# Kernel tuning notes

Hardware: AMD Instinct MI355X
Metric: run time of the kernel (lower is better)

Reference implementation:

```python
import jax, jax.numpy as jnp
import numpy as np
from jax import lax

B, T, N = 512, 512, 64  # batch, max_seq_len, num_tags


def setup_inputs() -> dict:
    key = jax.random.key(0)
    k1, k2, k3, k4 = jax.random.split(key, 4)
    inputs = jax.random.normal(k1, (B, T, N), dtype=jnp.float32)
    transition_params = jax.random.normal(k2, (N, N), dtype=jnp.float32)
    tag_indices = jax.random.randint(k3, (B, T), 0, N, dtype=jnp.int32)
    sequence_lengths = jax.random.randint(k4, (B,), 0, T, dtype=jnp.int32)
    return {
        "inputs": inputs,
        "transition_params": transition_params,
        "tag_indices": tag_indices,
        "sequence_lengths": sequence_lengths,
    }


def _crf_log_norm(inputs, transition_params, sequence_lengths):
    # inputs: [B, T, N]
    first = inputs[:, 0, :]                       # alpha after first token, [B, N]
    rest = jnp.transpose(inputs[:, 1:, :], (1, 0, 2))  # [T-1, B, N]

    def step(alpha, emit):
        # alpha: [B, N] -> broadcast-add transitions [N, N], logsumexp over prev tag
        new = emit + jax.nn.logsumexp(alpha[:, :, None] + transition_params[None], axis=1)
        return new, new

    _, alphas = lax.scan(step, first, rest)       # [T-1, B, N]
    all_alphas = jnp.concatenate([first[None], alphas], axis=0)  # [T, B, N]
    all_alphas = jnp.transpose(all_alphas, (1, 0, 2))            # [B, T, N]
    last_index = jnp.maximum(0, sequence_lengths - 1)            # [B]
    alpha_last = jnp.take_along_axis(all_alphas, last_index[:, None, None], axis=1)[:, 0, :]
    return jax.nn.logsumexp(alpha_last, axis=1)   # [B]


def _crf_sequence_score(inputs, tag_indices, sequence_lengths, transition_params):
    mask = (jnp.arange(T)[None, :] < sequence_lengths[:, None]).astype(inputs.dtype)  # [B, T]
    # unary: gather emission score of the gold tag at each position
    unary = jnp.take_along_axis(inputs, tag_indices[:, :, None], axis=2)[:, :, 0]      # [B, T]
    unary_scores = jnp.sum(unary * mask, axis=1)
    # binary: transition scores between consecutive gold tags
    binary = transition_params[tag_indices[:, :-1], tag_indices[:, 1:]]                # [B, T-1]
    binary_scores = jnp.sum(binary * mask[:, 1:], axis=1)
    return unary_scores + binary_scores


def reference(inputs, transition_params, tag_indices, sequence_lengths):
    tag_indices = tag_indices.astype(jnp.int32)
    sequence_lengths = sequence_lengths.astype(jnp.int32)
    sequence_scores = _crf_sequence_score(inputs, tag_indices, sequence_lengths, transition_params)
    log_norm = _crf_log_norm(inputs, transition_params, sequence_lengths)
    log_likelihood = sequence_scores - log_norm   # [B]
    return (log_likelihood, transition_params)
```

## Files before the change

kernel.cpp:

```cpp
#include <hip/hip_runtime.h>

#define BB 512
#define TT 512
#define NN 64

__device__ __forceinline__ float readlane_f(float v, int lane) {
    return __int_as_float(__builtin_amdgcn_readlane(__float_as_int(v), lane));
}

template<int BASE>
__device__ __forceinline__ float dot16(float p, const float4& A, const float4& B,
                                       const float4& C, const float4& D) {
    float s0 = readlane_f(p, BASE + 0) * A.x;
    float s1 = readlane_f(p, BASE + 1) * A.y;
    float s2 = readlane_f(p, BASE + 2) * A.z;
    float s3 = readlane_f(p, BASE + 3) * A.w;
    s0 = fmaf(readlane_f(p, BASE + 4),  B.x, s0);
    s1 = fmaf(readlane_f(p, BASE + 5),  B.y, s1);
    s2 = fmaf(readlane_f(p, BASE + 6),  B.z, s2);
    s3 = fmaf(readlane_f(p, BASE + 7),  B.w, s3);
    s0 = fmaf(readlane_f(p, BASE + 8),  C.x, s0);
    s1 = fmaf(readlane_f(p, BASE + 9),  C.y, s1);
    s2 = fmaf(readlane_f(p, BASE + 10), C.z, s2);
    s3 = fmaf(readlane_f(p, BASE + 11), C.w, s3);
    s0 = fmaf(readlane_f(p, BASE + 12), D.x, s0);
    s1 = fmaf(readlane_f(p, BASE + 13), D.y, s1);
    s2 = fmaf(readlane_f(p, BASE + 14), D.z, s2);
    s3 = fmaf(readlane_f(p, BASE + 15), D.w, s3);
    return (s0 + s1) + (s2 + s3);
}

template<int BASE>
__device__ __forceinline__ float run_loop(const float* __restrict__ inb,
                                          const float* __restrict__ trans,
                                          int last, int j, float alpha,
                                          float (*pbuf)[4][NN]) {
    constexpr int W = BASE / 16;

    float4 E0, E1, E2, E3;
    E0.x = __expf(trans[(BASE + 0) * NN + j]);
    E0.y = __expf(trans[(BASE + 1) * NN + j]);
    E0.z = __expf(trans[(BASE + 2) * NN + j]);
    E0.w = __expf(trans[(BASE + 3) * NN + j]);
    E1.x = __expf(trans[(BASE + 4) * NN + j]);
    E1.y = __expf(trans[(BASE + 5) * NN + j]);
    E1.z = __expf(trans[(BASE + 6) * NN + j]);
    E1.w = __expf(trans[(BASE + 7) * NN + j]);
    E2.x = __expf(trans[(BASE + 8) * NN + j]);
    E2.y = __expf(trans[(BASE + 9) * NN + j]);
    E2.z = __expf(trans[(BASE + 10) * NN + j]);
    E2.w = __expf(trans[(BASE + 11) * NN + j]);
    E3.x = __expf(trans[(BASE + 12) * NN + j]);
    E3.y = __expf(trans[(BASE + 13) * NN + j]);
    E3.z = __expf(trans[(BASE + 14) * NN + j]);
    E3.w = __expf(trans[(BASE + 15) * NN + j]);

    for (int t0 = 1; t0 <= last; t0 += 16) {
        float4 pf0, pf1, pf2, pf3;
#define LDE(vec, comp, r) { const int tc = (t0 + (r) <= last) ? (t0 + (r)) : last; \
                            vec.comp = inb[tc * NN + j]; }
        LDE(pf0, x, 0)  LDE(pf0, y, 1)  LDE(pf0, z, 2)  LDE(pf0, w, 3)
        LDE(pf1, x, 4)  LDE(pf1, y, 5)  LDE(pf1, z, 6)  LDE(pf1, w, 7)
        LDE(pf2, x, 8)  LDE(pf2, y, 9)  LDE(pf2, z, 10) LDE(pf2, w, 11)
        LDE(pf3, x, 12) LDE(pf3, y, 13) LDE(pf3, z, 14) LDE(pf3, w, 15)
#undef LDE

#define STEP(r, EM) { \
        const int tc = t0 + (r); \
        const float m = readlane_f(alpha, 0); \
        const float p = __expf(alpha - m); \
        const float partial = dot16<BASE>(p, E0, E1, E2, E3); \
        pbuf[tc & 1][W][j] = partial; \
        __syncthreads(); \
        const float* pb = &pbuf[tc & 1][0][0]; \
        const float s = (pb[0 * NN + j] + pb[1 * NN + j]) \
                      + (pb[2 * NN + j] + pb[3 * NN + j]); \
        if (tc <= last) alpha = (EM + m) + __logf(s); \
    }
        STEP(0,  pf0.x) STEP(1,  pf0.y) STEP(2,  pf0.z) STEP(3,  pf0.w)
        STEP(4,  pf1.x) STEP(5,  pf1.y) STEP(6,  pf1.z) STEP(7,  pf1.w)
        STEP(8,  pf2.x) STEP(9,  pf2.y) STEP(10, pf2.z) STEP(11, pf2.w)
        STEP(12, pf3.x) STEP(13, pf3.y) STEP(14, pf3.z) STEP(15, pf3.w)
#undef STEP
    }
    return alpha;
}

__global__ __launch_bounds__(256, 4) void crf_kernel(
    const float* __restrict__ inputs,
    const float* __restrict__ trans,
    const int*   __restrict__ tags,
    const int*   __restrict__ lens,
    float*       __restrict__ out)
{
    const int b   = blockIdx.x;
    const int tid = threadIdx.x;
    const int w   = tid >> 6;
    const int j   = tid & 63;

    if (b < 16) out[BB + b * 256 + tid] = trans[b * 256 + tid];

    const int L    = lens[b];
    const int last = (L - 1) > 0 ? (L - 1) : 0;

    const float* inb  = inputs + (size_t)b * TT * NN;
    const int*   tagb = tags + b * TT;

    __shared__ __align__(16) float pbuf[2][4][NN];
    __shared__ float scw[4];

    float sc = 0.f;
    #pragma unroll
    for (int k = 0; k < 2; ++k) {
        const int t  = tid + k * 256;
        const int tg = tagb[t];
        if (t < L) sc += inb[t * NN + tg];
        if (t + 1 < L) sc += trans[tg * NN + tagb[t + 1]];
    }
    #pragma unroll
    for (int x = 32; x >= 1; x >>= 1) sc += __shfl_xor(sc, x, 64);
    if (j == 0) scw[w] = sc;

    float alpha = inb[j];

    switch (w) {
        case 0:  alpha = run_loop<0>(inb, trans, last, j, alpha, pbuf);  break;
        case 1:  alpha = run_loop<16>(inb, trans, last, j, alpha, pbuf); break;
        case 2:  alpha = run_loop<32>(inb, trans, last, j, alpha, pbuf); break;
        default: alpha = run_loop<48>(inb, trans, last, j, alpha, pbuf); break;
    }

    __syncthreads();

    if (w == 0) {
        float mm = alpha;
        #pragma unroll
        for (int x = 32; x >= 1; x >>= 1) mm = fmaxf(mm, __shfl_xor(mm, x, 64));
        float e = __expf(alpha - mm);
        #pragma unroll
        for (int x = 32; x >= 1; x >>= 1) e += __shfl_xor(e, x, 64);
        if (j == 0) {
            const float lognorm = mm + __logf(e);
            out[b] = ((scw[0] + scw[1]) + (scw[2] + scw[3])) - lognorm;
        }
    }
}

extern "C" void kernel_launch(void* const* d_in, const int* in_sizes, int n_in,
                              void* d_out, int out_size, void* d_ws, size_t ws_size,
                              hipStream_t stream) {
    const float* inputs = (const float*)d_in[0];
    const float* trans  = (const float*)d_in[1];
    const int*   tags   = (const int*)d_in[2];
    const int*   lens   = (const int*)d_in[3];
    float*       out    = (float*)d_out;

    crf_kernel<<<dim3(BB), dim3(256), 0, stream>>>(inputs, trans, tags, lens, out);
}
```

Before: 241.0 us.

## Use one wavefront per sequence and drop cross-wave LDS reduction

Replaces the four-wave split of the 64x64 transition dot product with a single 64-lane wave that holds all 64 exp(transition) columns in registers and computes the full dot per step via readlanes. This removes the per-timestep __syncthreads and LDS partial-sum exchange that serialized each recurrence step. Emission loads are double-buffered in 16-step chunks, prefetching the next chunk while the current one is processed. The cost is four times more serial readlane/FMA work per wave per step and heavy register use for 64 floats of E.

New measurement: 227.7 us. -5.5%, faster.

```diff
diff --git a/kernel.cpp b/kernel.cpp
--- a/kernel.cpp
+++ b/kernel.cpp
@@ -8,142 +8,103 @@
     return __int_as_float(__builtin_amdgcn_readlane(__float_as_int(v), lane));
 }
 
-template<int BASE>
-__device__ __forceinline__ float dot16(float p, const float4& A, const float4& B,
-                                       const float4& C, const float4& D) {
-    float s0 = readlane_f(p, BASE + 0) * A.x;
-    float s1 = readlane_f(p, BASE + 1) * A.y;
-    float s2 = readlane_f(p, BASE + 2) * A.z;
-    float s3 = readlane_f(p, BASE + 3) * A.w;
-    s0 = fmaf(readlane_f(p, BASE + 4),  B.x, s0);
-    s1 = fmaf(readlane_f(p, BASE + 5),  B.y, s1);
-    s2 = fmaf(readlane_f(p, BASE + 6),  B.z, s2);
-    s3 = fmaf(readlane_f(p, BASE + 7),  B.w, s3);
-    s0 = fmaf(readlane_f(p, BASE + 8),  C.x, s0);
-    s1 = fmaf(readlane_f(p, BASE + 9),  C.y, s1);
-    s2 = fmaf(readlane_f(p, BASE + 10), C.z, s2);
-    s3 = fmaf(readlane_f(p, BASE + 11), C.w, s3);
-    s0 = fmaf(readlane_f(p, BASE + 12), D.x, s0);
-    s1 = fmaf(readlane_f(p, BASE + 13), D.y, s1);
-    s2 = fmaf(readlane_f(p, BASE + 14), D.z, s2);
-    s3 = fmaf(readlane_f(p, BASE + 15), D.w, s3);
+__device__ __forceinline__ float dot64(float p, const float4* E) {
+    float s0 = readlane_f(p, 0) * E[0].x;
+    float s1 = readlane_f(p, 1) * E[0].y;
+    float s2 = readlane_f(p, 2) * E[0].z;
+    float s3 = readlane_f(p, 3) * E[0].w;
+    #pragma unroll
+    for (int g = 1; g < 16; ++g) {
+        s0 = fmaf(readlane_f(p, 4 * g + 0), E[g].x, s0);
+        s1 = fmaf(readlane_f(p, 4 * g + 1), E[g].y, s1);
+        s2 = fmaf(readlane_f(p, 4 * g + 2), E[g].z, s2);
+        s3 = fmaf(readlane_f(p, 4 * g + 3), E[g].w, s3);
+    }
     return (s0 + s1) + (s2 + s3);
 }
 
-template<int BASE>
-__device__ __forceinline__ float run_loop(const float* __restrict__ inb,
-                                          const float* __restrict__ trans,
-                                          int last, int j, float alpha,
-                                          float (*pbuf)[4][NN]) {
-    constexpr int W = BASE / 16;
-
-    float4 E0, E1, E2, E3;
-    E0.x = __expf(trans[(BASE + 0) * NN + j]);
-    E0.y = __expf(trans[(BASE + 1) * NN + j]);
-    E0.z = __expf(trans[(BASE + 2) * NN + j]);
-    E0.w = __expf(trans[(BASE + 3) * NN + j]);
-    E1.x = __expf(trans[(BASE + 4) * NN + j]);
-    E1.y = __expf(trans[(BASE + 5) * NN + j]);
-    E1.z = __expf(trans[(BASE + 6) * NN + j]);
-    E1.w = __expf(trans[(BASE + 7) * NN + j]);
-    E2.x = __expf(trans[(BASE + 8) * NN + j]);
-    E2.y = __expf(trans[(BASE + 9) * NN + j]);
-    E2.z = __expf(trans[(BASE + 10) * NN + j]);
-    E2.w = __expf(trans[(BASE + 11) * NN + j]);
-    E3.x = __expf(trans[(BASE + 12) * NN + j]);
-    E3.y = __expf(trans[(BASE + 13) * NN + j]);
-    E3.z = __expf(trans[(BASE + 14) * NN + j]);
-    E3.w = __expf(trans[(BASE + 15) * NN + j]);
-
-    for (int t0 = 1; t0 <= last; t0 += 16) {
-        float4 pf0, pf1, pf2, pf3;
-#define LDE(vec, comp, r) { const int tc = (t0 + (r) <= last) ? (t0 + (r)) : last; \
-                            vec.comp = inb[tc * NN + j]; }
-        LDE(pf0, x, 0)  LDE(pf0, y, 1)  LDE(pf0, z, 2)  LDE(pf0, w, 3)
-        LDE(pf1, x, 4)  LDE(pf1, y, 5)  LDE(pf1, z, 6)  LDE(pf1, w, 7)
-        LDE(pf2, x, 8)  LDE(pf2, y, 9)  LDE(pf2, z, 10) LDE(pf2, w, 11)
-        LDE(pf3, x, 12) LDE(pf3, y, 13) LDE(pf3, z, 14) LDE(pf3, w, 15)
-#undef LDE
-
-#define STEP(r, EM) { \
-        const int tc = t0 + (r); \
-        const float m = readlane_f(alpha, 0); \
-        const float p = __expf(alpha - m); \
-        const float partial = dot16<BASE>(p, E0, E1, E2, E3); \
-        pbuf[tc & 1][W][j] = partial; \
-        __syncthreads(); \
-        const float* pb = &pbuf[tc & 1][0][0]; \
-        const float s = (pb[0 * NN + j] + pb[1 * NN + j]) \
-                      + (pb[2 * NN + j] + pb[3 * NN + j]); \
-        if (tc <= last) alpha = (EM + m) + __logf(s); \
-    }
-        STEP(0,  pf0.x) STEP(1,  pf0.y) STEP(2,  pf0.z) STEP(3,  pf0.w)
-        STEP(4,  pf1.x) STEP(5,  pf1.y) STEP(6,  pf1.z) STEP(7,  pf1.w)
-        STEP(8,  pf2.x) STEP(9,  pf2.y) STEP(10, pf2.z) STEP(11, pf2.w)
-        STEP(12, pf3.x) STEP(13, pf3.y) STEP(14, pf3.z) STEP(15, pf3.w)
-#undef STEP
-    }
-    return alpha;
-}
-
-__global__ __launch_bounds__(256, 4) void crf_kernel(
+__global__ __launch_bounds__(64, 1) void crf_kernel(
     const float* __restrict__ inputs,
     const float* __restrict__ trans,
     const int*   __restrict__ tags,
     const int*   __restrict__ lens,
     float*       __restrict__ out)
 {
-    const int b   = blockIdx.x;
-    const int tid = threadIdx.x;
-    const int w   = tid >> 6;
-    const int j   = tid & 63;
+    const int b = blockIdx.x;
+    const int j = threadIdx.x;
 
-    if (b < 16) out[BB + b * 256 + tid] = trans[b * 256 + tid];
+    if (b < 64) out[BB + b * 64 + j] = trans[b * 64 + j];
 
     const int L    = lens[b];
     const int last = (L - 1) > 0 ? (L - 1) : 0;
 
     const float* inb  = inputs + (size_t)b * TT * NN;
-    const int*   tagb = tags + b * TT;
-
-    __shared__ __align__(16) float pbuf[2][4][NN];
-    __shared__ float scw[4];
+    const int*   tagb = tags + (size_t)b * TT;
 
     float sc = 0.f;
     #pragma unroll
-    for (int k = 0; k < 2; ++k) {
-        const int t  = tid + k * 256;
+    for (int k = 0; k < 8; ++k) {
+        const int t  = k * 64 + j;
         const int tg = tagb[t];
         if (t < L) sc += inb[t * NN + tg];
         if (t + 1 < L) sc += trans[tg * NN + tagb[t + 1]];
     }
     #pragma unroll
     for (int x = 32; x >= 1; x >>= 1) sc += __shfl_xor(sc, x, 64);
-    if (j == 0) scw[w] = sc;
+
+    float4 E[16];
+    #pragma unroll
+    for (int g = 0; g < 16; ++g) {
+        E[g].x = __expf(trans[(4 * g + 0) * NN + j]);
+        E[g].y = __expf(trans[(4 * g + 1) * NN + j]);
+        E[g].z = __expf(trans[(4 * g + 2) * NN + j]);
+        E[g].w = __expf(trans[(4 * g + 3) * NN + j]);
+    }
 
     float alpha = inb[j];
 
-    switch (w) {
-        case 0:  alpha = run_loop<0>(inb, trans, last, j, alpha, pbuf);  break;
-        case 1:  alpha = run_loop<16>(inb, trans, last, j, alpha, pbuf); break;
-        case 2:  alpha = run_loop<32>(inb, trans, last, j, alpha, pbuf); break;
-        default: alpha = run_loop<48>(inb, trans, last, j, alpha, pbuf); break;
+    float4 pA0, pA1, pA2, pA3, pB0, pB1, pB2, pB3;
+
+#define LD(vec, comp, tt) { const int tc_ = (tt) <= last ? (tt) : last; \
+                            vec.comp = inb[tc_ * NN + j]; }
+#define LOADCHUNK(v0, v1, v2, v3, base) \
+    LD(v0, x, (base) + 0)  LD(v0, y, (base) + 1)  LD(v0, z, (base) + 2)  LD(v0, w, (base) + 3)  \
+    LD(v1, x, (base) + 4)  LD(v1, y, (base) + 5)  LD(v1, z, (base) + 6)  LD(v1, w, (base) + 7)  \
+    LD(v2, x, (base) + 8)  LD(v2, y, (base) + 9)  LD(v2, z, (base) + 10) LD(v2, w, (base) + 11) \
+    LD(v3, x, (base) + 12) LD(v3, y, (base) + 13) LD(v3, z, (base) + 14) LD(v3, w, (base) + 15)
+
+#define STEP(tc_, EM) { \
+    const float m = readlane_f(alpha, 0); \
+    const float p = __expf(alpha - m); \
+    const float s = dot64(p, E); \
+    if ((tc_) <= last) alpha = ((EM) + m) + __logf(s); \
+}
+
+    LOADCHUNK(pA0, pA1, pA2, pA3, 1)
+
+    for (int t0 = 1; t0 <= last; t0 += 32) {
+        LOADCHUNK(pB0, pB1, pB2, pB3, t0 + 16)
+        STEP(t0 + 0,  pA0.x) STEP(t0 + 1,  pA0.y) STEP(t0 + 2,  pA0.z) STEP(t0 + 3,  pA0.w)
+        STEP(t0 + 4,  pA1.x) STEP(t0 + 5,  pA1.y) STEP(t0 + 6,  pA1.z) STEP(t0 + 7,  pA1.w)
+        STEP(t0 + 8,  pA2.x) STEP(t0 + 9,  pA2.y) STEP(t0 + 10, pA2.z) STEP(t0 + 11, pA2.w)
+        STEP(t0 + 12, pA3.x) STEP(t0 + 13, pA3.y) STEP(t0 + 14, pA3.z) STEP(t0 + 15, pA3.w)
+        LOADCHUNK(pA0, pA1, pA2, pA3, t0 + 32)
+        STEP(t0 + 16, pB0.x) STEP(t0 + 17, pB0.y) STEP(t0 + 18, pB0.z) STEP(t0 + 19, pB0.w)
+        STEP(t0 + 20, pB1.x) STEP(t0 + 21, pB1.y) STEP(t0 + 22, pB1.z) STEP(t0 + 23, pB1.w)
+        STEP(t0 + 24, pB2.x) STEP(t0 + 25, pB2.y) STEP(t0 + 26, pB2.z) STEP(t0 + 27, pB2.w)
+        STEP(t0 + 28, pB3.x) STEP(t0 + 29, pB3.y) STEP(t0 + 30, pB3.z) STEP(t0 + 31, pB3.w)
     }
+#undef STEP
+#undef LOADCHUNK
+#undef LD
 
-    __syncthreads();
-
-    if (w == 0) {
-        float mm = alpha;
-        #pragma unroll
-        for (int x = 32; x >= 1; x >>= 1) mm = fmaxf(mm, __shfl_xor(mm, x, 64));
-        float e = __expf(alpha - mm);
-        #pragma unroll
-        for (int x = 32; x >= 1; x >>= 1) e += __shfl_xor(e, x, 64);
-        if (j == 0) {
-            const float lognorm = mm + __logf(e);
-            out[b] = ((scw[0] + scw[1]) + (scw[2] + scw[3])) - lognorm;
-        }
-    }
+    float mm = alpha;
+    #pragma unroll
+    for (int x = 32; x >= 1; x >>= 1) mm = fmaxf(mm, __shfl_xor(mm, x, 64));
+    float e = __expf(alpha - mm);
+    #pragma unroll
+    for (int x = 32; x >= 1; x >>= 1) e += __shfl_xor(e, x, 64);
+    if (j == 0) out[b] = sc - (mm + __logf(e));
 }
 
 extern "C" void kernel_launch(void* const* d_in, const int* in_sizes, int n_in,
@@ -155,5 +116,5 @@
     const int*   lens   = (const int*)d_in[3];
     float*       out    = (float*)d_out;
 
-    crf_kernel<<<dim3(BB), dim3(256), 0, stream>>>(inputs, trans, tags, lens, out);
+    crf_kernel<<<dim3(BB), dim3(64), 0, stream>>>(inputs, trans, tags, lens, out);
 }
```
